# Performance work log

Hardware: AMD Instinct MI355X
Metric: run time of the kernel (lower is better)

Reference implementation:

```python
import jax, jax.numpy as jnp
import numpy as np

N, C, HID, FEAT = 4096, 1024, 512, 128
KS = (5, 10, 15)  # k values used when k == -1 (hyedge_concat path)


def _sq_cdist(x):
    # squared pairwise euclidean distances; monotone in torch.cdist for topk
    n = (x * x).sum(-1)
    d2 = n[:, None] + n[None, :] - 2.0 * (x @ x.T)
    return jnp.maximum(d2, 0.0)


def neighbor_distance(x, k):
    # k nearest neighbors (smallest distance, self included) -> incidence H [N, N]
    # hyperedge e (column) = neighborhood of node e
    _, idx = jax.lax.top_k(-_sq_cdist(x), k)  # [N, k]
    n = x.shape[0]
    H = jnp.zeros((n, n), x.dtype).at[idx, jnp.arange(n)[:, None]].set(1.0)
    return H


def build_H(x, k):
    if k == -1:  # k is a static Python int
        return jnp.concatenate([neighbor_distance(x, kk) for kk in KS], axis=1)
    return neighbor_distance(x, k)


def hyconv(x, H, W):
    Dv = H.sum(1)  # node degree [N]
    De = H.sum(0)  # edge degree [E]
    dv = jnp.where(Dv > 0, 1.0 / jnp.sqrt(Dv), 0.0)
    de = jnp.where(De > 0, 1.0 / De, 0.0)
    m = (H.T @ (x * dv[:, None])) * de[:, None]  # [E, C]
    return ((H @ m) * dv[:, None]) @ W


def feat_model(x, H, W1, W2):
    return hyconv(jax.nn.relu(hyconv(x, H, W1)), H, W2)


def setup_inputs() -> dict:
    key = jax.random.key(0)
    k1, k2, k3, k4 = jax.random.split(key, 4)
    return {
        "fts_gt": jax.random.normal(k1, (N, C), jnp.float32),
        "fts1": jax.random.normal(k2, (N, C), jnp.float32),
        "W1": jax.random.normal(k3, (C, HID), jnp.float32) / np.sqrt(C).astype(np.float32),
        "W2": jax.random.normal(k4, (HID, FEAT), jnp.float32) / np.sqrt(HID).astype(np.float32),
        "k": -1,
    }


def reference(fts_gt, fts1, W1, W2, k):
    H_gt = build_H(fts_gt, k)
    H1 = build_H(fts1, k)
    feat_gt = feat_model(fts_gt, H_gt, W1, W2)  # [N, FEAT]
    feat1 = feat_model(fts1, H1, W1, W2)
    # sensitive == 'attribute': mean over node dim
    feat_gt = feat_gt.mean(axis=0)
    feat1 = feat1.mean(axis=0)
    y0 = feat_gt.sum()
    y1 = feat1.sum()
    y_compare = (feat_gt[None] - feat1[None]).sum()[None]  # shape [1]
    return (jax.nn.sigmoid(y_compare), y0, y1)
```

## Files before the change

kernel.cpp:

```cpp
#include <hip/hip_runtime.h>
#include <math.h>


#define NN   4096
#define CC   1024
#define HIDN 512
#define FEATN 128
#define NE   12288
#define KTOT 30
#define KMAX 15
#define CH   16
#define MAXCH (NN + NN * KTOT / CH)

typedef __attribute__((ext_vector_type(4))) int i32x4;
typedef unsigned short ushort_t;

__device__ __forceinline__ unsigned short bf16_rne(float x) {
    unsigned u = __float_as_uint(x);
    unsigned r = (u + 0x7FFFu + ((u >> 16) & 1u)) >> 16;
    return (unsigned short)r;
}
__device__ __forceinline__ float bf16_lo(unsigned u) { return __uint_as_float(u << 16); }
__device__ __forceinline__ float bf16_hi(unsigned u) { return __uint_as_float(u & 0xFFFF0000u); }
__device__ __forceinline__ unsigned packbf(float a, float b) {
    return (unsigned)bf16_rne(a) | ((unsigned)bf16_rne(b) << 16);
}

__device__ __forceinline__ void async16(void* lds, const void* g) {
    __builtin_amdgcn_global_load_lds((const __attribute__((address_space(1))) unsigned int*)g,
                                     (__attribute__((address_space(3))) unsigned int*)lds, 16, 0, 0);
}

__global__ __launch_bounds__(256) void k_rownorm2(const float* __restrict__ X,
                                                  float* __restrict__ nrm,
                                                  float* __restrict__ qs) {
    __shared__ float s[256];
    __shared__ float sm[256];
    int i = blockIdx.x, t = threadIdx.x;
    const float* row = X + (size_t)i * CC;
    float acc = 0.f, mx = 0.f;
#pragma unroll
    for (int j = 0; j < CC / 256; ++j) {
        float v = row[t + 256 * j];
        acc += v * v;
        mx = fmaxf(mx, fabsf(v));
    }
    s[t] = acc; sm[t] = mx; __syncthreads();
    for (int d = 128; d > 0; d >>= 1) {
        if (t < d) { s[t] += s[t + d]; sm[t] = fmaxf(sm[t], sm[t + d]); }
        __syncthreads();
    }
    if (t == 0) { nrm[i] = s[0]; qs[i] = fmaxf(sm[0], 1e-20f) / 127.0f; }
}

__global__ __launch_bounds__(256) void k_quant(const float* __restrict__ X,
                                               const float* __restrict__ qs,
                                               signed char* __restrict__ H,
                                               signed char* __restrict__ L) {
    int p = blockIdx.x * 256 + threadIdx.x;
    int i = p >> 8;
    float inv = 1.0f / qs[i];
    float4 v = *reinterpret_cast<const float4*>(&X[(size_t)p * 4]);
    float f[4] = { v.x, v.y, v.z, v.w };
    char hh[4], ll[4];
#pragma unroll
    for (int j = 0; j < 4; ++j) {
        float xs = f[j] * inv;
        float h = rintf(xs);
        float l = rintf((xs - h) * 128.0f);
        hh[j] = (char)(int)h;
        ll[j] = (char)(int)l;
    }
    *reinterpret_cast<char4*>(&H[(size_t)p * 4]) = make_char4(hh[0], hh[1], hh[2], hh[3]);
    *reinterpret_cast<char4*>(&L[(size_t)p * 4]) = make_char4(ll[0], ll[1], ll[2], ll[3]);
}

__global__ __launch_bounds__(256) void k_w1max(const float* __restrict__ W,
                                               unsigned* __restrict__ sigb) {
    int t = threadIdx.x;
    int r0 = blockIdx.x * 64;
    float m0 = 0.f, m1 = 0.f;
    for (int r = 0; r < 64; ++r) {
        const float* row = W + (size_t)(r0 + r) * HIDN;
        m0 = fmaxf(m0, fabsf(row[t]));
        m1 = fmaxf(m1, fabsf(row[t + 256]));
    }
    atomicMax(&sigb[t],       __float_as_uint(m0));
    atomicMax(&sigb[t + 256], __float_as_uint(m1));
}

__global__ __launch_bounds__(256) void k_sig(const unsigned* __restrict__ sigb,
                                             float* __restrict__ sig) {
    int i = blockIdx.x * 256 + threadIdx.x;
    sig[i] = fmaxf(__uint_as_float(sigb[i]), 1e-20f) / 127.0f;
}

__global__ __launch_bounds__(256) void k_wt8(const float* __restrict__ W,
                                             const float* __restrict__ sig,
                                             signed char* __restrict__ Th,
                                             signed char* __restrict__ Tl) {
    __shared__ float s[32][33];
    int bx = blockIdx.x, by = blockIdx.y;
    int tx = threadIdx.x & 31, ty = threadIdx.x >> 5;
#pragma unroll
    for (int rr = 0; rr < 4; ++rr) {
        int k = by * 32 + ty + rr * 8;
        s[ty + rr * 8][tx] = W[(size_t)k * HIDN + bx * 32 + tx];
    }
    __syncthreads();
#pragma unroll
    for (int rr = 0; rr < 4; ++rr) {
        int n = bx * 32 + ty + rr * 8;
        int k = by * 32 + tx;
        float x = s[tx][ty + rr * 8];
        float xs = x / sig[n];
        float h = rintf(xs);
        float l = rintf((xs - h) * 128.0f);
        Th[(size_t)n * CC + k] = (char)(int)h;
        Tl[(size_t)n * CC + k] = (char)(int)l;
    }
}

__global__ __launch_bounds__(256) void k_w2bar(const float* __restrict__ W2,
                                               float* __restrict__ wbar) {
    int k = blockIdx.x * 256 + threadIdx.x;
    const float* row = W2 + (size_t)k * FEATN;
    float s = 0.f;
#pragma unroll
    for (int f = 0; f < FEATN; f += 4) {
        float4 v = *reinterpret_cast<const float4*>(&row[f]);
        s += v.x + v.y + v.z + v.w;
    }
    wbar[k] = s;
}

template <bool SYM, bool OUTB>
__global__ __launch_bounds__(256) void k_mm8(const signed char* __restrict__ Ah,
                                             const signed char* __restrict__ Al,
                                             const signed char* __restrict__ Bh,
                                             const signed char* __restrict__ Bl,
                                             const float* __restrict__ rs,
                                             const float* __restrict__ cs,
                                             float* __restrict__ C,
                                             ushort_t* __restrict__ Cb, int ldc) {
    int bi, bj;
    if (SYM) {
        int b0 = (int)blockIdx.x;
        int L = (b0 & 7) * 66 + (b0 >> 3);
        int rem = L, si = 0;
        for (; si < 8; ++si) {
            int grp = 10 + (7 - si) * 16;
            if (rem < grp) break;
            rem -= grp;
        }
        int sj, u, v;
        if (rem < 10) {
            int uu = 0, r2 = rem;
            while (r2 >= 4 - uu) { r2 -= 4 - uu; ++uu; }
            u = uu; v = uu + r2; sj = si;
        } else {
            int r2 = rem - 10;
            sj = si + 1 + (r2 >> 4);
            int w2 = r2 & 15;
            u = w2 >> 2; v = w2 & 3;
        }
        bi = si * 4 + u; bj = sj * 4 + v;
    } else {
        bi = blockIdx.y; bj = blockIdx.x;
    }
    __shared__ char smem[2][4][128][64];
    int t = threadIdx.x;
    int w = t >> 6, l = t & 63;
    int wr = (w >> 1) * 64, wc = (w & 1) * 64;

    i32x4 acc1[4][4], acc2[4][4];
#pragma unroll
    for (int i = 0; i < 4; ++i)
#pragma unroll
        for (int j = 0; j < 4; ++j) { acc1[i][j] = (i32x4){0,0,0,0}; acc2[i][j] = (i32x4){0,0,0,0}; }

    const signed char* src[4] = {
        Ah + (size_t)bi * 128 * 1024,
        Al + (size_t)bi * 128 * 1024,
        Bh + (size_t)bj * 128 * 1024,
        Bl + (size_t)bj * 128 * 1024
    };
    int srow = l >> 2;
    int sslot = (l & 3) ^ ((l >> 3) & 3);

    int col = l & 15;
    int kg = l >> 4;

    auto stage = [&](int buf, int kt) {
        int k0 = kt * 64;
#pragma unroll
        for (int q = 0; q < 4; ++q) {
#pragma unroll
            for (int s2 = 0; s2 < 2; ++s2) {
                int rbase = (w * 2 + s2) * 16;
                const signed char* g = src[q] + (size_t)(rbase + srow) * 1024 + k0 + sslot * 16;
                async16(&smem[buf][q][rbase][0], g);
            }
        }
    };

    stage(0, 0);
    __syncthreads();
    int cur = 0;
    for (int kt = 0; kt < 16; ++kt) {
        if (kt + 1 < 16) stage(cur ^ 1, kt + 1);
        i32x4 ah[4], al4[4], bh4[4], bl4[4];
#pragma unroll
        for (int mi = 0; mi < 4; ++mi) {
            int row = wr + mi * 16 + col;
            int ph = kg ^ ((row >> 1) & 3);
            ah[mi]  = *reinterpret_cast<const i32x4*>(&smem[cur][0][row][ph * 16]);
            al4[mi] = *reinterpret_cast<const i32x4*>(&smem[cur][1][row][ph * 16]);
        }
#pragma unroll
        for (int nj = 0; nj < 4; ++nj) {
            int row = wc + nj * 16 + col;
            int ph = kg ^ ((row >> 1) & 3);
            bh4[nj] = *reinterpret_cast<const i32x4*>(&smem[cur][2][row][ph * 16]);
            bl4[nj] = *reinterpret_cast<const i32x4*>(&smem[cur][3][row][ph * 16]);
        }
#pragma unroll
        for (int mi = 0; mi < 4; ++mi)
#pragma unroll
            for (int nj = 0; nj < 4; ++nj) {
                acc1[mi][nj] = __builtin_amdgcn_mfma_i32_16x16x64_i8(ah[mi], bh4[nj], acc1[mi][nj], 0, 0, 0);
                acc2[mi][nj] = __builtin_amdgcn_mfma_i32_16x16x64_i8(ah[mi], bl4[nj], acc2[mi][nj], 0, 0, 0);
                acc2[mi][nj] = __builtin_amdgcn_mfma_i32_16x16x64_i8(al4[mi], bh4[nj], acc2[mi][nj], 0, 0, 0);
            }
        __syncthreads();
        cur ^= 1;
    }

#pragma unroll
    for (int mi = 0; mi < 4; ++mi) {
        int rg0 = bi * 128 + wr + mi * 16 + (l >> 4) * 4;
#pragma unroll
        for (int nj = 0; nj < 4; ++nj) {
            int cg = bj * 128 + wc + nj * 16 + col;
            float csv = cs[cg];
            float vr[4];
#pragma unroll
            for (int r = 0; r < 4; ++r)
                vr[r] = ((float)acc1[mi][nj][r] + (float)acc2[mi][nj][r] * (1.0f / 128.0f))
                        * rs[rg0 + r] * csv;
            if (OUTB) {
#pragma unroll
                for (int r = 0; r < 4; ++r)
                    Cb[(size_t)(rg0 + r) * ldc + cg] = bf16_rne(vr[r]);
            } else {
#pragma unroll
                for (int r = 0; r < 4; ++r)
                    C[(size_t)(rg0 + r) * ldc + cg] = vr[r];
                if (SYM && bi != bj)
                    *reinterpret_cast<float4*>(&C[(size_t)cg * ldc + rg0]) =
                        make_float4(vr[0], vr[1], vr[2], vr[3]);
            }
        }
    }
}

__global__ __launch_bounds__(256) void k_topk(const float* __restrict__ G,
                                              const float* __restrict__ nrm,
                                              int* __restrict__ idx_out) {
    __shared__ unsigned long long wsm[4];
    int e = blockIdx.x, t = threadIdx.x;
    float ne = nrm[e];
    const float* Grow = G + (size_t)e * NN;
    unsigned long long key[16];
    unsigned long long my = ~0ull;
#pragma unroll
    for (int j = 0; j < 16; ++j) {
        int i = t + 256 * j;
        float v = fmaxf(ne + nrm[i] - 2.0f * Grow[i], 0.0f);
        unsigned long long k = ((unsigned long long)__float_as_uint(v) << 32) | (unsigned)i;
        key[j] = k;
        my = k < my ? k : my;
    }
    for (int r = 0; r < KMAX; ++r) {
        unsigned long long m = my;
#pragma unroll
        for (int d = 1; d < 64; d <<= 1) {
            unsigned long long o = __shfl_xor(m, d);
            m = o < m ? o : m;
        }
        if ((t & 63) == 0) wsm[t >> 6] = m;
        __syncthreads();
        unsigned long long b0 = wsm[0] < wsm[1] ? wsm[0] : wsm[1];
        unsigned long long b1 = wsm[2] < wsm[3] ? wsm[2] : wsm[3];
        unsigned long long bk = b0 < b1 ? b0 : b1;
        int win = (int)(unsigned)bk;
        if (t == 0) idx_out[e * 16 + r] = win;
        if (t == (win & 255)) {
            int jw = win >> 8;
#pragma unroll
            for (int jj = 0; jj < 16; ++jj) if (jj == jw) key[jj] = ~0ull;
            my = ~0ull;
#pragma unroll
            for (int jj = 0; jj < 16; ++jj) my = key[jj] < my ? key[jj] : my;
        }
        __syncthreads();
    }
}

__device__ __forceinline__ void decode_pair(int p, int& e, int& b, int& j) {
    e = p / KTOT;
    int q = p - e * KTOT;
    if (q < 5)       { b = 0; j = q; }
    else if (q < 15) { b = 1; j = q - 5; }
    else             { b = 2; j = q - 15; }
}

__global__ __launch_bounds__(256) void k_count(const int* __restrict__ idx, int* __restrict__ Dv) {
    int p = blockIdx.x * 256 + threadIdx.x;
    int e, b, j; decode_pair(p, e, b, j);
    (void)b;
    atomicAdd(&Dv[idx[e * 16 + j]], 1);
}

__global__ __launch_bounds__(256) void k_dv(const int* __restrict__ Dv,
                                            const float* __restrict__ qs,
                                            float* __restrict__ dvv,
                                            float* __restrict__ rs1) {
    int i = blockIdx.x * 256 + threadIdx.x;
    int d = Dv[i];
    float dv = d > 0 ? 1.0f / sqrtf((float)d) : 0.0f;
    dvv[i] = dv;
    rs1[i] = dv * qs[i];
}

__global__ __launch_bounds__(1024) void k_scan(const int* __restrict__ Dv,
                                               int* __restrict__ offs,
                                               int* __restrict__ cur,
                                               int* __restrict__ chunkoffs,
                                               int* __restrict__ nchunks) {
    __shared__ int s[1024];
    int t = threadIdx.x;
    int v[4]; int sum = 0;
#pragma unroll
    for (int j = 0; j < 4; ++j) { v[j] = Dv[t * 4 + j]; sum += v[j]; }
    s[t] = sum; __syncthreads();
    for (int d = 1; d < 1024; d <<= 1) {
        int add = (t >= d) ? s[t - d] : 0;
        __syncthreads();
        s[t] += add;
        __syncthreads();
    }
    int run = s[t] - sum;
#pragma unroll
    for (int j = 0; j < 4; ++j) { offs[t * 4 + j] = run; cur[t * 4 + j] = run; run += v[j]; }
    if (t == 1023) offs[NN] = run;
    __syncthreads();
    int c[4]; int csum = 0;
#pragma unroll
    for (int j = 0; j < 4; ++j) { c[j] = (v[j] + CH - 1) / CH; csum += c[j]; }
    s[t] = csum; __syncthreads();
    for (int d = 1; d < 1024; d <<= 1) {
        int add = (t >= d) ? s[t - d] : 0;
        __syncthreads();
        s[t] += add;
        __syncthreads();
    }
    int crun = s[t] - csum;
#pragma unroll
    for (int j = 0; j < 4; ++j) { chunkoffs[t * 4 + j] = crun; crun += c[j]; }
    if (t == 1023) { chunkoffs[NN] = crun; *nchunks = crun; }
}

__global__ __launch_bounds__(256) void k_fill(const int* __restrict__ idx,
                                              int* __restrict__ cur,
                                              int* __restrict__ adj) {
    int p = blockIdx.x * 256 + threadIdx.x;
    int e, b, j; decode_pair(p, e, b, j);
    int i = idx[e * 16 + j];
    int eg = b * NN + e;
    int pos = atomicAdd(&cur[i], 1);
    adj[pos] = eg;
}

__global__ __launch_bounds__(256) void k_tasks(const int* __restrict__ chunkoffs,
                                               int* __restrict__ task_node) {
    int i = blockIdx.x * 256 + threadIdx.x;
    int c0 = chunkoffs[i], c1 = chunkoffs[i + 1];
    for (int c = c0; c < c1; ++c) task_node[c] = i;
}

__global__ __launch_bounds__(256) void k_ze(const int* __restrict__ idx,
                                            const float* __restrict__ dvv,
                                            float* __restrict__ ze) {
    int eg = blockIdx.x * 256 + threadIdx.x;
    int b = eg >> 12, e = eg & (NN - 1);
    int kb = (b == 0) ? 5 : (b == 1) ? 10 : 15;
    const int* row = idx + e * 16;
    float s = 0.f;
    for (int j = 0; j < kb; ++j) s += dvv[row[j]];
    ze[eg] = s / (float)kb;
}

__global__ __launch_bounds__(256) void k_ascat(const int* __restrict__ idx,
                                               const float* __restrict__ ze,
                                               float* __restrict__ a) {
    int p = blockIdx.x * 256 + threadIdx.x;
    int e, b, j; decode_pair(p, e, b, j);
    atomicAdd(&a[idx[e * 16 + j]], ze[b * NN + e]);
}

__global__ __launch_bounds__(256) void k_edge3(const int* __restrict__ idx,
                                               const ushort_t* __restrict__ t1b,
                                               ushort_t* __restrict__ m) {
    int p = blockIdx.x * 256 + threadIdx.x;
    int e = p >> 6;
    int c8 = (p & 63) * 8;
    const int* row = idx + e * 16;
    float acc[8] = {};
    auto addrow = [&](int j) {
        uint4 raw = *reinterpret_cast<const uint4*>(&t1b[(size_t)row[j] * HIDN + c8]);
        acc[0] += bf16_lo(raw.x); acc[1] += bf16_hi(raw.x);
        acc[2] += bf16_lo(raw.y); acc[3] += bf16_hi(raw.y);
        acc[4] += bf16_lo(raw.z); acc[5] += bf16_hi(raw.z);
        acc[6] += bf16_lo(raw.w); acc[7] += bf16_hi(raw.w);
    };
    auto store = [&](size_t eg, float sc) {
        uint4 o;
        o.x = packbf(acc[0] * sc, acc[1] * sc);
        o.y = packbf(acc[2] * sc, acc[3] * sc);
        o.z = packbf(acc[4] * sc, acc[5] * sc);
        o.w = packbf(acc[6] * sc, acc[7] * sc);
        *reinterpret_cast<uint4*>(&m[eg * HIDN + c8]) = o;
    };
#pragma unroll
    for (int j = 0; j < 5; ++j) addrow(j);
    store((size_t)e, 0.2f);
#pragma unroll
    for (int j = 5; j < 10; ++j) addrow(j);
    store((size_t)(NN + e), 0.1f);
#pragma unroll
    for (int j = 10; j < 15; ++j) addrow(j);
    store((size_t)(2 * NN + e), 1.0f / 15.0f);
}

__global__ __launch_bounds__(256) void k_chunk(const int* __restrict__ offs,
                                               const int* __restrict__ chunkoffs,
                                               const int* __restrict__ task_node,
                                               const int* __restrict__ nchunks,
                                               const int* __restrict__ adj,
                                               const ushort_t* __restrict__ m,
                                               float* __restrict__ partial) {
    int task = blockIdx.x * 4 + threadIdx.x / 64;
    if (task >= *nchunks) return;
    int c8 = (threadIdx.x & 63) * 8;
    int i = task_node[task];
    int ck = task - chunkoffs[i];
    int q0 = offs[i] + ck * CH;
    int n = offs[i + 1] - q0;
    n = n < CH ? n : CH;
    int e[CH];
#pragma unroll
    for (int j = 0; j < CH; ++j) e[j] = (j < n) ? adj[q0 + j] : -1;
    float acc[8] = {};
#pragma unroll
    for (int j = 0; j < CH; ++j) {
        if (e[j] >= 0) {
            uint4 raw = *reinterpret_cast<const uint4*>(&m[(size_t)e[j] * HIDN + c8]);
            acc[0] += bf16_lo(raw.x); acc[1] += bf16_hi(raw.x);
            acc[2] += bf16_lo(raw.y); acc[3] += bf16_hi(raw.y);
            acc[4] += bf16_lo(raw.z); acc[5] += bf16_hi(raw.z);
            acc[6] += bf16_lo(raw.w); acc[7] += bf16_hi(raw.w);
        }
    }
    float* o = &partial[(size_t)task * HIDN + c8];
    *reinterpret_cast<float4*>(o)     = make_float4(acc[0], acc[1], acc[2], acc[3]);
    *reinterpret_cast<float4*>(o + 4) = make_float4(acc[4], acc[5], acc[6], acc[7]);
}

__global__ __launch_bounds__(256) void k_comb2(const int* __restrict__ chunkoffs,
                                               const float* __restrict__ dvv,
                                               const float* __restrict__ a,
                                               const float* __restrict__ wbar,
                                               const float* __restrict__ partial,
                                               float* __restrict__ g) {
    __shared__ float s[256];
    int p = blockIdx.x * 256 + threadIdx.x;
    int i = p >> 7;
    int c4 = (p & 127) * 4;
    int c0 = chunkoffs[i], c1 = chunkoffs[i + 1];
    float4 acc = make_float4(0.f, 0.f, 0.f, 0.f);
    for (int c = c0; c < c1; ++c) {
        float4 v = *reinterpret_cast<const float4*>(&partial[(size_t)c * HIDN + c4]);
        acc.x += v.x; acc.y += v.y; acc.z += v.z; acc.w += v.w;
    }
    float dv = dvv[i];
    float4 wv = *reinterpret_cast<const float4*>(&wbar[c4]);
    float val = fmaxf(acc.x * dv, 0.f) * wv.x + fmaxf(acc.y * dv, 0.f) * wv.y +
                fmaxf(acc.z * dv, 0.f) * wv.z + fmaxf(acc.w * dv, 0.f) * wv.w;
    int t = threadIdx.x;
    s[t] = val; __syncthreads();
    for (int d = 64; d > 0; d >>= 1) {
        if ((t & 127) < d) s[t] += s[t + d];
        __syncthreads();
    }
    if ((t & 127) == 0) g[i] = s[t] * dv * a[i];
}

__global__ __launch_bounds__(1024) void k_yred(const float* __restrict__ g,
                                               float* __restrict__ ys, int slot) {
    __shared__ float s[1024];
    int t = threadIdx.x;
    s[t] = g[t] + g[t + 1024] + g[t + 2048] + g[t + 3072];
    __syncthreads();
    for (int d = 512; d > 0; d >>= 1) { if (t < d) s[t] += s[t + d]; __syncthreads(); }
    if (t == 0) ys[slot] = s[0];
}

__global__ void k_fin(const float* __restrict__ ys, float* __restrict__ out) {
    float y0 = ys[0] / (float)NN, y1 = ys[1] / (float)NN;
    out[0] = 1.0f / (1.0f + expf(-(y0 - y1)));
    out[1] = y0;
    out[2] = y1;
}

extern "C" void kernel_launch(void* const* d_in, const int* in_sizes, int n_in,
                              void* d_out, int out_size, void* d_ws, size_t ws_size,
                              hipStream_t stream) {
    const float* fts[2] = { (const float*)d_in[0], (const float*)d_in[1] };
    const float* W1 = (const float*)d_in[2];
    const float* W2 = (const float*)d_in[3];
    float* out = (float*)d_out;

    char* p = (char*)d_ws;
    auto alloc = [&](size_t b) { char* r = p; p += (b + 255) & ~(size_t)255; return r; };
    float* G    = (float*)alloc((size_t)NN * NN * 4);
    float* nrm  = (float*)alloc((size_t)NN * 4);
    float* qs   = (float*)alloc((size_t)NN * 4);
    int*   idx  = (int*)  alloc((size_t)NN * 16 * 4);
    int*   Dv   = (int*)  alloc((size_t)NN * 4);
    float* dvv  = (float*)alloc((size_t)NN * 4);
    float* rs1  = (float*)alloc((size_t)NN * 4);
    int*   offs = (int*)  alloc((size_t)(NN + 1) * 4);
    int*   cur  = (int*)  alloc((size_t)NN * 4);
    int*   coffs= (int*)  alloc((size_t)(NN + 1) * 4);
    int*   nch  = (int*)  alloc(4);
    int*   tnode= (int*)  alloc((size_t)MAXCH * 4);
    int*   adj  = (int*)  alloc((size_t)NN * KTOT * 4);
    signed char* Xqh = (signed char*)alloc((size_t)NN * CC);
    signed char* Xql = (signed char*)alloc((size_t)NN * CC);
    signed char* Wqh = (signed char*)alloc((size_t)HIDN * CC);
    signed char* Wql = (signed char*)alloc((size_t)HIDN * CC);
    unsigned* sigb   = (unsigned*)alloc((size_t)HIDN * 4);
    float* w1sig = (float*)alloc((size_t)HIDN * 4);
    ushort_t* t1b = (ushort_t*)alloc((size_t)NN * HIDN * 2);
    ushort_t* m   = (ushort_t*)alloc((size_t)NE * HIDN * 2);
    float* wbar = (float*)alloc((size_t)HIDN * 4);
    float* ze   = (float*)alloc((size_t)NE * 4);
    float* a    = (float*)alloc((size_t)NN * 4);
    float* g    = (float*)alloc((size_t)NN * 4);
    float* ys   = (float*)alloc(2 * 4);

    float* partial = G;

    hipMemsetAsync(sigb, 0, HIDN * 4, stream);
    k_w1max<<<CC / 64, 256, 0, stream>>>(W1, sigb);
    k_sig<<<HIDN / 256, 256, 0, stream>>>(sigb, w1sig);
    k_wt8<<<dim3(HIDN / 32, CC / 32), 256, 0, stream>>>(W1, w1sig, Wqh, Wql);
    k_w2bar<<<HIDN / 256, 256, 0, stream>>>(W2, wbar);

    for (int s = 0; s < 2; ++s) {
        const float* X = fts[s];
        k_rownorm2<<<NN, 256, 0, stream>>>(X, nrm, qs);
        k_quant<<<NN * CC / 4 / 256, 256, 0, stream>>>(X, qs, Xqh, Xql);
        k_mm8<true, false><<<528, 256, 0, stream>>>(Xqh, Xql, Xqh, Xql, qs, qs, G, nullptr, NN);
        k_topk<<<NN, 256, 0, stream>>>(G, nrm, idx);
        hipMemsetAsync(Dv, 0, NN * 4, stream);
        k_count<<<NN * KTOT / 256, 256, 0, stream>>>(idx, Dv);
        k_dv<<<NN / 256, 256, 0, stream>>>(Dv, qs, dvv, rs1);
        k_scan<<<1, 1024, 0, stream>>>(Dv, offs, cur, coffs, nch);
        k_fill<<<NN * KTOT / 256, 256, 0, stream>>>(idx, cur, adj);
        k_tasks<<<NN / 256, 256, 0, stream>>>(coffs, tnode);
        k_ze<<<NE / 256, 256, 0, stream>>>(idx, dvv, ze);
        hipMemsetAsync(a, 0, NN * 4, stream);
        k_ascat<<<NN * KTOT / 256, 256, 0, stream>>>(idx, ze, a);
        k_mm8<false, true><<<dim3(HIDN / 128, NN / 128), 256, 0, stream>>>(Xqh, Xql, Wqh, Wql, rs1, w1sig, nullptr, t1b, HIDN);
        k_edge3<<<NN * 64 / 256, 256, 0, stream>>>(idx, t1b, m);
        k_chunk<<<(MAXCH + 3) / 4, 256, 0, stream>>>(offs, coffs, tnode, nch, adj, m, partial);
        k_comb2<<<NN * 128 / 256, 256, 0, stream>>>(coffs, dvv, a, wbar, partial, g);
        k_yred<<<1, 1024, 0, stream>>>(g, ys, s);
    }
    k_fin<<<1, 1, 0, stream>>>(ys, out);
}
```

Before: 594.3 us.

## Fuse small preprocessing kernels and vectorize top-k distance loads

Merges row-norm and quantization into one kernel so each input row is read once. Folds the degree-normalization and task-node fill into the single-block scan kernel, and merges edge mean and scatter into one kernel. In top-k, each thread now reads 16 contiguous distances through float4 loads, and the winner-to-thread mapping is updated to match. This cuts launches per branch and removes an extra pass over the inputs, at the cost of more serial work inside the single-block scan and a different atomic pattern.

```diff
diff --git a/kernel.cpp b/kernel.cpp
--- a/kernel.cpp
+++ b/kernel.cpp
@@ -31,36 +31,26 @@
                                      (__attribute__((address_space(3))) unsigned int*)lds, 16, 0, 0);
 }
 
-__global__ __launch_bounds__(256) void k_rownorm2(const float* __restrict__ X,
-                                                  float* __restrict__ nrm,
-                                                  float* __restrict__ qs) {
+__global__ __launch_bounds__(256) void k_rowprep(const float* __restrict__ X,
+                                                 float* __restrict__ nrm,
+                                                 float* __restrict__ qs,
+                                                 signed char* __restrict__ H,
+                                                 signed char* __restrict__ L) {
     __shared__ float s[256];
     __shared__ float sm[256];
     int i = blockIdx.x, t = threadIdx.x;
     const float* row = X + (size_t)i * CC;
-    float acc = 0.f, mx = 0.f;
-#pragma unroll
-    for (int j = 0; j < CC / 256; ++j) {
-        float v = row[t + 256 * j];
-        acc += v * v;
-        mx = fmaxf(mx, fabsf(v));
-    }
+    float4 v = *reinterpret_cast<const float4*>(&row[t * 4]);
+    float acc = v.x * v.x + v.y * v.y + v.z * v.z + v.w * v.w;
+    float mx = fmaxf(fmaxf(fabsf(v.x), fabsf(v.y)), fmaxf(fabsf(v.z), fabsf(v.w)));
     s[t] = acc; sm[t] = mx; __syncthreads();
     for (int d = 128; d > 0; d >>= 1) {
         if (t < d) { s[t] += s[t + d]; sm[t] = fmaxf(sm[t], sm[t + d]); }
         __syncthreads();
     }
-    if (t == 0) { nrm[i] = s[0]; qs[i] = fmaxf(sm[0], 1e-20f) / 127.0f; }
-}
-
-__global__ __launch_bounds__(256) void k_quant(const float* __restrict__ X,
-                                               const float* __restrict__ qs,
-                                               signed char* __restrict__ H,
-                                               signed char* __restrict__ L) {
-    int p = blockIdx.x * 256 + threadIdx.x;
-    int i = p >> 8;
-    float inv = 1.0f / qs[i];
-    float4 v = *reinterpret_cast<const float4*>(&X[(size_t)p * 4]);
+    float q = fmaxf(sm[0], 1e-20f) / 127.0f;
+    if (t == 0) { nrm[i] = s[0]; qs[i] = q; }
+    float inv = 1.0f / q;
     float f[4] = { v.x, v.y, v.z, v.w };
     char hh[4], ll[4];
 #pragma unroll
@@ -71,8 +61,8 @@
         hh[j] = (char)(int)h;
         ll[j] = (char)(int)l;
     }
-    *reinterpret_cast<char4*>(&H[(size_t)p * 4]) = make_char4(hh[0], hh[1], hh[2], hh[3]);
-    *reinterpret_cast<char4*>(&L[(size_t)p * 4]) = make_char4(ll[0], ll[1], ll[2], ll[3]);
+    *reinterpret_cast<char4*>(&H[(size_t)i * CC + t * 4]) = make_char4(hh[0], hh[1], hh[2], hh[3]);
+    *reinterpret_cast<char4*>(&L[(size_t)i * CC + t * 4]) = make_char4(ll[0], ll[1], ll[2], ll[3]);
 }
 
 __global__ __launch_bounds__(256) void k_w1max(const float* __restrict__ W,
@@ -274,13 +264,22 @@
     unsigned long long key[16];
     unsigned long long my = ~0ull;
 #pragma unroll
-    for (int j = 0; j < 16; ++j) {
-        int i = t + 256 * j;
-        float v = fmaxf(ne + nrm[i] - 2.0f * Grow[i], 0.0f);
-        unsigned long long k = ((unsigned long long)__float_as_uint(v) << 32) | (unsigned)i;
-        key[j] = k;
-        my = k < my ? k : my;
-    }
+    for (int q = 0; q < 4; ++q) {
+        float4 gv = *reinterpret_cast<const float4*>(&Grow[t * 16 + q * 4]);
+        float4 nv = *reinterpret_cast<const float4*>(&nrm[t * 16 + q * 4]);
+        float d0 = fmaxf(ne + nv.x - 2.0f * gv.x, 0.0f);
+        float d1 = fmaxf(ne + nv.y - 2.0f * gv.y, 0.0f);
+        float d2 = fmaxf(ne + nv.z - 2.0f * gv.z, 0.0f);
+        float d3 = fmaxf(ne + nv.w - 2.0f * gv.w, 0.0f);
+        int i0 = t * 16 + q * 4;
+        key[q * 4 + 0] = ((unsigned long long)__float_as_uint(d0) << 32) | (unsigned)(i0 + 0);
+        key[q * 4 + 1] = ((unsigned long long)__float_as_uint(d1) << 32) | (unsigned)(i0 + 1);
+        key[q * 4 + 2] = ((unsigned long long)__float_as_uint(d2) << 32) | (unsigned)(i0 + 2);
+        key[q * 4 + 3] = ((unsigned long long)__float_as_uint(d3) << 32) | (unsigned)(i0 + 3);
+    }
+#pragma unroll
+    for (int j = 0; j < 16; ++j) my = key[j] < my ? key[j] : my;
+
     for (int r = 0; r < KMAX; ++r) {
         unsigned long long m = my;
 #pragma unroll
@@ -295,8 +294,8 @@
         unsigned long long bk = b0 < b1 ? b0 : b1;
         int win = (int)(unsigned)bk;
         if (t == 0) idx_out[e * 16 + r] = win;
-        if (t == (win & 255)) {
-            int jw = win >> 8;
+        if (t == (win >> 4)) {
+            int jw = win & 15;
 #pragma unroll
             for (int jj = 0; jj < 16; ++jj) if (jj == jw) key[jj] = ~0ull;
             my = ~0ull;
@@ -322,27 +321,27 @@
     atomicAdd(&Dv[idx[e * 16 + j]], 1);
 }
 
-__global__ __launch_bounds__(256) void k_dv(const int* __restrict__ Dv,
-                                            const float* __restrict__ qs,
-                                            float* __restrict__ dvv,
-                                            float* __restrict__ rs1) {
-    int i = blockIdx.x * 256 + threadIdx.x;
-    int d = Dv[i];
-    float dv = d > 0 ? 1.0f / sqrtf((float)d) : 0.0f;
-    dvv[i] = dv;
-    rs1[i] = dv * qs[i];
-}
-
 __global__ __launch_bounds__(1024) void k_scan(const int* __restrict__ Dv,
+                                               const float* __restrict__ qs,
+                                               float* __restrict__ dvv,
+                                               float* __restrict__ rs1,
                                                int* __restrict__ offs,
                                                int* __restrict__ cur,
                                                int* __restrict__ chunkoffs,
-                                               int* __restrict__ nchunks) {
+                                               int* __restrict__ nchunks,
+                                               int* __restrict__ tnode) {
     __shared__ int s[1024];
     int t = threadIdx.x;
     int v[4]; int sum = 0;
 #pragma unroll
     for (int j = 0; j < 4; ++j) { v[j] = Dv[t * 4 + j]; sum += v[j]; }
+#pragma unroll
+    for (int j = 0; j < 4; ++j) {
+        int i = t * 4 + j;
+        float dv = v[j] > 0 ? 1.0f / sqrtf((float)v[j]) : 0.0f;
+        dvv[i] = dv;
+        rs1[i] = dv * qs[i];
+    }
     s[t] = sum; __syncthreads();
     for (int d = 1; d < 1024; d <<= 1) {
         int add = (t >= d) ? s[t - d] : 0;
@@ -367,7 +366,11 @@
     }
     int crun = s[t] - csum;
 #pragma unroll
-    for (int j = 0; j < 4; ++j) { chunkoffs[t * 4 + j] = crun; crun += c[j]; }
+    for (int j = 0; j < 4; ++j) {
+        chunkoffs[t * 4 + j] = crun;
+        for (int q = 0; q < c[j]; ++q) tnode[crun + q] = t * 4 + j;
+        crun += c[j];
+    }
     if (t == 1023) { chunkoffs[NN] = crun; *nchunks = crun; }
 }
 
@@ -382,31 +385,17 @@
     adj[pos] = eg;
 }
 
-__global__ __launch_bounds__(256) void k_tasks(const int* __restrict__ chunkoffs,
-                                               int* __restrict__ task_node) {
-    int i = blockIdx.x * 256 + threadIdx.x;
-    int c0 = chunkoffs[i], c1 = chunkoffs[i + 1];
-    for (int c = c0; c < c1; ++c) task_node[c] = i;
-}
-
-__global__ __launch_bounds__(256) void k_ze(const int* __restrict__ idx,
-                                            const float* __restrict__ dvv,
-                                            float* __restrict__ ze) {
+__global__ __launch_bounds__(256) void k_zescat(const int* __restrict__ idx,
+                                                const float* __restrict__ dvv,
+                                                float* __restrict__ a) {
     int eg = blockIdx.x * 256 + threadIdx.x;
     int b = eg >> 12, e = eg & (NN - 1);
     int kb = (b == 0) ? 5 : (b == 1) ? 10 : 15;
     const int* row = idx + e * 16;
     float s = 0.f;
     for (int j = 0; j < kb; ++j) s += dvv[row[j]];
-    ze[eg] = s / (float)kb;
-}
-
-__global__ __launch_bounds__(256) void k_ascat(const int* __restrict__ idx,
-                                               const float* __restrict__ ze,
-                                               float* __restrict__ a) {
-    int p = blockIdx.x * 256 + threadIdx.x;
-    int e, b, j; decode_pair(p, e, b, j);
-    atomicAdd(&a[idx[e * 16 + j]], ze[b * NN + e]);
+    float ze = s / (float)kb;
+    for (int j = 0; j < kb; ++j) atomicAdd(&a[row[j]], ze);
 }
 
 __global__ __launch_bounds__(256) void k_edge3(const int* __restrict__ idx,
@@ -555,7 +544,6 @@
     ushort_t* t1b = (ushort_t*)alloc((size_t)NN * HIDN * 2);
     ushort_t* m   = (ushort_t*)alloc((size_t)NE * HIDN * 2);
     float* wbar = (float*)alloc((size_t)HIDN * 4);
-    float* ze   = (float*)alloc((size_t)NE * 4);
     float* a    = (float*)alloc((size_t)NN * 4);
     float* g    = (float*)alloc((size_t)NN * 4);
     float* ys   = (float*)alloc(2 * 4);
@@ -570,19 +558,15 @@
 
     for (int s = 0; s < 2; ++s) {
         const float* X = fts[s];
-        k_rownorm2<<<NN, 256, 0, stream>>>(X, nrm, qs);
-        k_quant<<<NN * CC / 4 / 256, 256, 0, stream>>>(X, qs, Xqh, Xql);
+        k_rowprep<<<NN, 256, 0, stream>>>(X, nrm, qs, Xqh, Xql);
         k_mm8<true, false><<<528, 256, 0, stream>>>(Xqh, Xql, Xqh, Xql, qs, qs, G, nullptr, NN);
         k_topk<<<NN, 256, 0, stream>>>(G, nrm, idx);
         hipMemsetAsync(Dv, 0, NN * 4, stream);
         k_count<<<NN * KTOT / 256, 256, 0, stream>>>(idx, Dv);
-        k_dv<<<NN / 256, 256, 0, stream>>>(Dv, qs, dvv, rs1);
-        k_scan<<<1, 1024, 0, stream>>>(Dv, offs, cur, coffs, nch);
+        k_scan<<<1, 1024, 0, stream>>>(Dv, qs, dvv, rs1, offs, cur, coffs, nch, tnode);
         k_fill<<<NN * KTOT / 256, 256, 0, stream>>>(idx, cur, adj);
-        k_tasks<<<NN / 256, 256, 0, stream>>>(coffs, tnode);
-        k_ze<<<NE / 256, 256, 0, stream>>>(idx, dvv, ze);
         hipMemsetAsync(a, 0, NN * 4, stream);
-        k_ascat<<<NN * KTOT / 256, 256, 0, stream>>>(idx, ze, a);
+        k_zescat<<<NE / 256, 256, 0, stream>>>(idx, dvv, a);
         k_mm8<false, true><<<dim3(HIDN / 128, NN / 128), 256, 0, stream>>>(Xqh, Xql, Wqh, Wql, rs1, w1sig, nullptr, t1b, HIDN);
         k_edge3<<<NN * 64 / 256, 256, 0, stream>>>(idx, t1b, m);
         k_chunk<<<(MAXCH + 3) / 4, 256, 0, stream>>>(offs, coffs, tnode, nch, adj, m, partial);
```

New measurement: 595.0 us, median of 2. Within noise of the previous version (+0.1%).
